# Kernel optimization log

Measured on AMD Instinct MI355X. Metric: run time of the kernel, lower is better.

The kernel has to match this reference:

```python
import jax, jax.numpy as jnp
import numpy as np

ALPHA = 0.2  # leakyrelu negative slope
NEG_INF = -1.0e12


def setup_inputs() -> dict:
    key = jax.random.key(0)
    k1, k2, k3, k4, k5 = jax.random.split(key, 5)
    B, N, C_in, C_out = 8, 2048, 256, 256
    inp = jax.random.normal(k1, (B, N, C_in), dtype=jnp.float32)
    adj = jax.random.randint(k2, (N, N), 0, 2, dtype=jnp.int32)
    # xavier_uniform with gain=1.414 for (C_in, C_out)
    limit = 1.414 * np.sqrt(6.0 / (C_in + C_out))
    W1 = jax.random.uniform(k3, (C_in, C_out), jnp.float32, -limit, limit)
    W2 = jax.random.uniform(k4, (C_in, C_out), jnp.float32, -limit, limit)
    W3 = jax.random.uniform(k5, (C_in, C_out), jnp.float32, -limit, limit)
    return {"inp": inp, "adj": adj, "W1": W1, "W2": W2, "W3": W3}


def reference(inp, adj, W1, W2, W3):
    # inp: [B,N,Cin], adj: [N,N], W*: [Cin,Cout]
    h1 = jnp.einsum('bnc,cd->bnd', inp, W1)  # [B,N,Cout] queries
    h2 = jnp.einsum('bnc,cd->bnd', inp, W2)  # [B,N,Cout] keys
    h3 = jnp.einsum('bnc,cd->bnd', inp, W3)  # [B,N,Cout] values
    e = jnp.einsum('bnd,bmd->bnm', h1, h2)   # [B,N,N] scores
    e = jax.nn.leaky_relu(e, ALPHA)
    e = jnp.where(adj[None, :, :] > 0, e, NEG_INF)
    attention = jax.nn.softmax(e, axis=-1)   # dropout p=0 / eval mode -> identity
    h_prime = jnp.einsum('bnm,bmd->bnd', attention, h3)
    return jax.nn.relu(h_prime)  # concat=True
```

## Files before the change

### kernel.cpp

```cpp
#include <hip/hip_runtime.h>

typedef __bf16 bf16_t;
typedef __bf16 bf16x4 __attribute__((ext_vector_type(4)));
typedef __bf16 bf16x8 __attribute__((ext_vector_type(8)));
typedef float floatx4 __attribute__((ext_vector_type(4)));
typedef signed char i8_t;
typedef int intx4 __attribute__((ext_vector_type(4)));

__device__ inline void split_hl(float v, bf16_t& hi, bf16_t& lo) {
    hi = (bf16_t)v;
    lo = (bf16_t)(v - (float)hi);
}

__global__ void wtrans_kernel(const float* __restrict__ W1,
                              const float* __restrict__ W2,
                              const float* __restrict__ W3,
                              bf16_t* __restrict__ Wthi, bf16_t* __restrict__ Wtlo) {
    __shared__ float T[64 * 68];
    const int zi = blockIdx.z;
    const float* W = (zi == 0) ? W1 : ((zi == 1) ? W2 : W3);
    bf16_t* ohi = Wthi + zi * 256 * 256;
    bf16_t* olo = Wtlo + zi * 256 * 256;
    const int c0 = blockIdx.x * 64, d0 = blockIdx.y * 64;
    const int tid = threadIdx.x;
#pragma unroll
    for (int i = 0; i < 4; i++) {
        int idx = i * 256 + tid;
        int r = idx >> 4, c4 = (idx & 15) * 4;
        floatx4 v = *(const floatx4*)(W + (c0 + r) * 256 + d0 + c4);
        *(floatx4*)(&T[r * 68 + c4]) = v;
    }
    __syncthreads();
#pragma unroll
    for (int i = 0; i < 4; i++) {
        int idx = i * 256 + tid;
        int rd = idx & 63, cc4 = (idx >> 6) * 4;
        bf16x4 vh, vl;
#pragma unroll
        for (int ii = 0; ii < 4; ii++) {
            float v = T[(cc4 + ii) * 68 + rd];
            bf16_t h, l; split_hl(v, h, l);
            vh[ii] = h; vl[ii] = l;
        }
        *(bf16x4*)(ohi + (d0 + rd) * 256 + c0 + cc4) = vh;
        *(bf16x4*)(olo + (d0 + rd) * 256 + c0 + cc4) = vl;
    }
}

__global__ __launch_bounds__(256) void projadj_kernel(
    const float* __restrict__ X,
    const bf16_t* __restrict__ Wthi, const bf16_t* __restrict__ Wtlo,
    i8_t* __restrict__ Q8h, i8_t* __restrict__ Q8l, float* __restrict__ sqv,
    i8_t* __restrict__ K8h, i8_t* __restrict__ K8l, float* __restrict__ skv,
    bf16_t* __restrict__ H3t,
    const int* __restrict__ adj, unsigned* __restrict__ bits) {
    __shared__ bf16_t Xh[64 * 40], Xl[64 * 40];
    __shared__ bf16_t Wh[256 * 40], Wl[256 * 40];
    __shared__ float amS[2][64];

    const int tid = threadIdx.x;
    const int blk = blockIdx.x;
    if (blk < 512) {
        int id = blk * 256 + tid;
        const int* p = adj + (size_t)id * 32;
        unsigned wbits = 0;
#pragma unroll
        for (int j = 0; j < 32; j += 4) {
            int4 v = *(const int4*)(p + j);
            wbits |= (v.x > 0 ? 1u : 0u) << j;
            wbits |= (v.y > 0 ? 1u : 0u) << (j + 1);
            wbits |= (v.z > 0 ? 1u : 0u) << (j + 2);
            wbits |= (v.w > 0 ? 1u : 0u) << (j + 3);
        }
        bits[id] = wbits;
        return;
    }

    const int pblk = blk - 512;
    const int z = pblk >> 8;
    const int row0 = (pblk & 255) * 64;
    const int w = tid >> 6, lane = tid & 63;
    const int m = lane & 15, q = lane >> 4;
    const int wr = w >> 1, wc = w & 1;
    const bf16_t* Wzh = Wthi + z * 256 * 256;
    const bf16_t* Wzl = Wtlo + z * 256 * 256;

    floatx4 acc[16];
#pragma unroll
    for (int i = 0; i < 16; i++) acc[i] = (floatx4){0.f, 0.f, 0.f, 0.f};

    for (int c0 = 0; c0 < 256; c0 += 32) {
#pragma unroll
        for (int i = 0; i < 2; i++) {
            int idx = i * 256 + tid;
            int r = idx >> 3, c4 = (idx & 7) * 4;
            floatx4 v = *(const floatx4*)(X + (size_t)(row0 + r) * 256 + c0 + c4);
            bf16x4 vh, vl;
#pragma unroll
            for (int ii = 0; ii < 4; ii++) {
                bf16_t h, l; split_hl(v[ii], h, l);
                vh[ii] = h; vl[ii] = l;
            }
            *(bf16x4*)(&Xh[r * 40 + c4]) = vh;
            *(bf16x4*)(&Xl[r * 40 + c4]) = vl;
        }
#pragma unroll
        for (int i = 0; i < 4; i++) {
            int idx = i * 256 + tid;
            int d = idx >> 2, c8 = (idx & 3) * 8;
            *(bf16x8*)(&Wh[d * 40 + c8]) = *(const bf16x8*)(Wzh + d * 256 + c0 + c8);
            *(bf16x8*)(&Wl[d * 40 + c8]) = *(const bf16x8*)(Wzl + d * 256 + c0 + c8);
        }
        __syncthreads();
        bf16x8 ah[2], al[2];
#pragma unroll
        for (int rt = 0; rt < 2; rt++) {
            ah[rt] = *(const bf16x8*)(&Xh[(wr * 32 + rt * 16 + m) * 40 + q * 8]);
            al[rt] = *(const bf16x8*)(&Xl[(wr * 32 + rt * 16 + m) * 40 + q * 8]);
        }
#pragma unroll
        for (int ct = 0; ct < 8; ct++) {
            bf16x8 bh = *(const bf16x8*)(&Wh[(wc * 128 + ct * 16 + m) * 40 + q * 8]);
            bf16x8 bl = *(const bf16x8*)(&Wl[(wc * 128 + ct * 16 + m) * 40 + q * 8]);
#pragma unroll
            for (int rt = 0; rt < 2; rt++) {
                acc[rt * 8 + ct] = __builtin_amdgcn_mfma_f32_16x16x32_bf16(ah[rt], bh, acc[rt * 8 + ct], 0, 0, 0);
                acc[rt * 8 + ct] = __builtin_amdgcn_mfma_f32_16x16x32_bf16(ah[rt], bl, acc[rt * 8 + ct], 0, 0, 0);
                acc[rt * 8 + ct] = __builtin_amdgcn_mfma_f32_16x16x32_bf16(al[rt], bh, acc[rt * 8 + ct], 0, 0, 0);
            }
        }
        __syncthreads();
    }

    if (z < 2) {
        i8_t* Dh = (z == 0) ? Q8h : K8h;
        i8_t* Dl = (z == 0) ? Q8l : K8l;
        float* sv = (z == 0) ? sqv : skv;
        float am[2][4];
#pragma unroll
        for (int rt = 0; rt < 2; rt++)
#pragma unroll
            for (int r = 0; r < 4; r++) am[rt][r] = 0.f;
#pragma unroll
        for (int ct = 0; ct < 8; ct++)
#pragma unroll
            for (int rt = 0; rt < 2; rt++)
#pragma unroll
                for (int r = 0; r < 4; r++)
                    am[rt][r] = fmaxf(am[rt][r], fabsf(acc[rt * 8 + ct][r]));
#pragma unroll
        for (int off = 1; off < 16; off <<= 1)
#pragma unroll
            for (int rt = 0; rt < 2; rt++)
#pragma unroll
                for (int r = 0; r < 4; r++)
                    am[rt][r] = fmaxf(am[rt][r], __shfl_xor(am[rt][r], off, 64));
        if (m == 0) {
#pragma unroll
            for (int rt = 0; rt < 2; rt++)
#pragma unroll
                for (int r = 0; r < 4; r++)
                    amS[wc][wr * 32 + rt * 16 + q * 4 + r] = am[rt][r];
        }
        __syncthreads();
        float sc[2][4], inv[2][4];
#pragma unroll
        for (int rt = 0; rt < 2; rt++)
#pragma unroll
            for (int r = 0; r < 4; r++) {
                int row = wr * 32 + rt * 16 + q * 4 + r;
                float a = fmaxf(amS[0][row], amS[1][row]);
                sc[rt][r]  = (a > 0.f) ? a * (1.f / 127.f) : 1.f;
                inv[rt][r] = (a > 0.f) ? 127.f / a : 0.f;
            }
#pragma unroll
        for (int ct = 0; ct < 8; ct++)
#pragma unroll
            for (int rt = 0; rt < 2; rt++)
#pragma unroll
                for (int r = 0; r < 4; r++) {
                    float vq = acc[rt * 8 + ct][r] * inv[rt][r];
                    float qh = rintf(vq);
                    float ql = fminf(fmaxf(rintf((vq - qh) * 256.f), -127.f), 127.f);
                    int offo = (row0 + wr * 32 + rt * 16 + q * 4 + r) * 256 +
                               wc * 128 + ct * 16 + m;
                    Dh[offo] = (i8_t)(int)qh;
                    Dl[offo] = (i8_t)(int)ql;
                }
        if (m == 0 && wc == 0) {
#pragma unroll
            for (int rt = 0; rt < 2; rt++)
#pragma unroll
                for (int r = 0; r < 4; r++)
                    sv[row0 + wr * 32 + rt * 16 + q * 4 + r] = sc[rt][r];
        }
    } else {
#pragma unroll
        for (int ct = 0; ct < 8; ct++)
#pragma unroll
            for (int rt = 0; rt < 2; rt++)
#pragma unroll
                for (int r = 0; r < 4; r++) {
                    int token = row0 + wr * 32 + rt * 16 + q * 4 + r;
                    int b = token >> 11, n = token & 2047;
                    H3t[(size_t)(b * 256 + wc * 128 + ct * 16 + m) * 2048 + n] =
                        (bf16_t)acc[rt * 8 + ct][r];
                }
    }
}

#define K8SW(row, off) ((off) ^ (((row) & 7) << 4))
#define VSW(row, off)  ((off) ^ ((((row) >> 1) & 3) << 4))
__global__ __launch_bounds__(256, 2) void attn_kernel(
    const i8_t* __restrict__ Q8h, const i8_t* __restrict__ Q8l,
    const float* __restrict__ sqv,
    const i8_t* __restrict__ K8h, const i8_t* __restrict__ K8l,
    const float* __restrict__ skv,
    const bf16_t* __restrict__ H3t, const unsigned* __restrict__ adjbits,
    bf16_t* __restrict__ Opart, float* __restrict__ mpart, float* __restrict__ lpart,
    int klen) {
    __shared__ i8_t K8[2][32 * 256];
    __shared__ bf16_t Vl[256 * 32];
    __shared__ bf16_t Pl[4][16 * 32];

    const int nwg = (int)(gridDim.x * gridDim.y * gridDim.z);
    const int wgid = (int)(blockIdx.x + (blockIdx.y << 5) + (blockIdx.z << 8));
    const int nid = (wgid & 7) * (nwg >> 3) + (wgid >> 3);
    const int qb = nid & 31;
    const int b  = (nid >> 5) & 7;
    const int kz = nid >> 8;

    const int q0 = qb * 64;
    const int tid = threadIdx.x;
    const int w = tid >> 6, lane = tid & 63;
    const int m = lane & 15, q = lane >> 4;

    char* K8B0 = (char*)&K8[0][0];
    char* K8B1 = (char*)&K8[1][0];
    char* VlB  = (char*)&Vl[0];
    char* PlB  = (char*)&Pl[w][0];

    const i8_t* qrh = Q8h + (size_t)(b * 2048 + q0 + w * 16 + m) * 256;
    const i8_t* qrl = Q8l + (size_t)(b * 2048 + q0 + w * 16 + m) * 256;
    intx4 qh8[4], ql8[4];
#pragma unroll
    for (int ck = 0; ck < 4; ck++) {
        qh8[ck] = *(const intx4*)(qrh + ck * 64 + q * 16);
        ql8[ck] = *(const intx4*)(qrl + ck * 64 + q * 16);
    }
    float sq4[4];
#pragma unroll
    for (int r = 0; r < 4; r++) sq4[r] = sqv[b * 2048 + q0 + w * 16 + q * 4 + r];

    bf16x8 vones;
#pragma unroll
    for (int i = 0; i < 8; i++) vones[i] = (bf16_t)1.0f;

    float m_run[4];
#pragma unroll
    for (int r = 0; r < 4; r++) m_run[r] = -3.0e38f;
    floatx4 l_acc = (floatx4){0.f, 0.f, 0.f, 0.f};
    floatx4 o[16];
#pragma unroll
    for (int i = 0; i < 16; i++) o[i] = (floatx4){0.f, 0.f, 0.f, 0.f};

    const unsigned* bitrow[4];
#pragma unroll
    for (int r = 0; r < 4; r++)
        bitrow[r] = adjbits + (size_t)(q0 + w * 16 + q * 4 + r) * 64;

    intx4 rkh[2], rkl[2];
    bf16x8 rvv[4];
    float skt[2], skn[2];
    const int kbeg = kz * klen, kend = kbeg + klen;

#pragma unroll
    for (int i = 0; i < 2; i++) {
        int ci = i * 256 + tid;
        int kr = ci >> 4, cb = (ci & 15) * 16;
        rkh[i] = *(const intx4*)(K8h + (size_t)(b * 2048 + kbeg + kr) * 256 + cb);
        rkl[i] = *(const intx4*)(K8l + (size_t)(b * 2048 + kbeg + kr) * 256 + cb);
    }
#pragma unroll
    for (int i = 0; i < 4; i++) {
        int ci = i * 256 + tid;
        int d = ci >> 2, k8 = (ci & 3) * 8;
        rvv[i] = *(const bf16x8*)(H3t + (size_t)(b * 256 + d) * 2048 + kbeg + k8);
    }
    skt[0] = skv[b * 2048 + kbeg + m];
    skt[1] = skv[b * 2048 + kbeg + 16 + m];

    for (int k0 = kbeg; k0 < kend; k0 += 32) {
        __syncthreads();
#pragma unroll
        for (int i = 0; i < 2; i++) {
            int ci = i * 256 + tid;
            int kr = ci >> 4, cb = (ci & 15) * 16;
            *(intx4*)(K8B0 + K8SW(kr, kr * 256 + cb)) = rkh[i];
            *(intx4*)(K8B1 + K8SW(kr, kr * 256 + cb)) = rkl[i];
        }
#pragma unroll
        for (int i = 0; i < 4; i++) {
            int ci = i * 256 + tid;
            int d = ci >> 2, kb = (ci & 3) * 16;
            *(bf16x8*)(VlB + VSW(d, d * 64 + kb)) = rvv[i];
        }
        __syncthreads();
        if (k0 + 32 < kend) {
            int kn = k0 + 32;
#pragma unroll
            for (int i = 0; i < 2; i++) {
                int ci = i * 256 + tid;
                int kr = ci >> 4, cb = (ci & 15) * 16;
                rkh[i] = *(const intx4*)(K8h + (size_t)(b * 2048 + kn + kr) * 256 + cb);
                rkl[i] = *(const intx4*)(K8l + (size_t)(b * 2048 + kn + kr) * 256 + cb);
            }
#pragma unroll
            for (int i = 0; i < 4; i++) {
                int ci = i * 256 + tid;
                int d = ci >> 2, k8 = (ci & 3) * 8;
                rvv[i] = *(const bf16x8*)(H3t + (size_t)(b * 256 + d) * 2048 + kn + k8);
            }
            skn[0] = skv[b * 2048 + kn + m];
            skn[1] = skv[b * 2048 + kn + 16 + m];
        }

        float s[2][4];
#pragma unroll
        for (int t = 0; t < 2; t++) {
            intx4 ch = {0, 0, 0, 0}, cm = {0, 0, 0, 0};
            const int row = t * 16 + m;
#pragma unroll
            for (int ck = 0; ck < 4; ck++) {
                const int cb2 = ck * 64 + q * 16;
                intx4 kh = *(const intx4*)(K8B0 + K8SW(row, row * 256 + cb2));
                intx4 kl = *(const intx4*)(K8B1 + K8SW(row, row * 256 + cb2));
                ch = __builtin_amdgcn_mfma_i32_16x16x64_i8(qh8[ck], kh, ch, 0, 0, 0);
                cm = __builtin_amdgcn_mfma_i32_16x16x64_i8(qh8[ck], kl, cm, 0, 0, 0);
                cm = __builtin_amdgcn_mfma_i32_16x16x64_i8(ql8[ck], kh, cm, 0, 0, 0);
            }
#pragma unroll
            for (int r = 0; r < 4; r++)
                s[t][r] = fmaf((float)cm[r], 0.00390625f, (float)ch[r]) * (sq4[r] * skt[t]);
        }

        unsigned aw[4];
#pragma unroll
        for (int r = 0; r < 4; r++) aw[r] = bitrow[r][k0 >> 5];
        float p[2][4], tmax[4];
#pragma unroll
        for (int r = 0; r < 4; r++) tmax[r] = -3.0e38f;
#pragma unroll
        for (int t = 0; t < 2; t++)
#pragma unroll
            for (int r = 0; r < 4; r++) {
                float v = s[t][r];
                v = (v > 0.f) ? v : 0.2f * v;
                v = ((aw[r] >> (t * 16 + m)) & 1u) ? v : -1.0e12f;
                p[t][r] = v;
                tmax[r] = fmaxf(tmax[r], v);
            }
#pragma unroll
        for (int off = 1; off < 16; off <<= 1)
#pragma unroll
            for (int r = 0; r < 4; r++)
                tmax[r] = fmaxf(tmax[r], __shfl_xor(tmax[r], off, 64));

        int rise = 0;
        float mnew[4];
#pragma unroll
        for (int r = 0; r < 4; r++) {
            mnew[r] = fmaxf(m_run[r], tmax[r]);
            rise |= (mnew[r] > m_run[r]);
        }
        if (__any(rise)) {
#pragma unroll
            for (int r = 0; r < 4; r++) {
                float alpha = __expf(m_run[r] - mnew[r]);
                m_run[r] = mnew[r];
                l_acc[r] *= alpha;
#pragma unroll
                for (int nt = 0; nt < 16; nt++) o[nt][r] *= alpha;
            }
        }
#pragma unroll
        for (int t = 0; t < 2; t++)
#pragma unroll
            for (int r = 0; r < 4; r++)
                p[t][r] = __expf(p[t][r] - m_run[r]);

#pragma unroll
        for (int t = 0; t < 2; t++)
#pragma unroll
            for (int r = 0; r < 4; r++) {
                int row = q * 4 + r;
                *(bf16_t*)(PlB + VSW(row, row * 64 + (t * 16 + m) * 2)) = (bf16_t)p[t][r];
            }
        bf16x8 pf = *(const bf16x8*)(PlB + VSW(m, m * 64 + q * 16));

        l_acc = __builtin_amdgcn_mfma_f32_16x16x32_bf16(pf, vones, l_acc, 0, 0, 0);

#pragma unroll
        for (int nt = 0; nt < 16; nt++) {
            const int vr = nt * 16 + m;
            bf16x8 vf = *(const bf16x8*)(VlB + VSW(vr, vr * 64 + q * 16));
            o[nt] = __builtin_amdgcn_mfma_f32_16x16x32_bf16(pf, vf, o[nt], 0, 0, 0);
        }
        skt[0] = skn[0];
        skt[1] = skn[1];
    }

    const int rowg = kz * 16384 + b * 2048 + q0 + w * 16 + q * 4;
#pragma unroll
    for (int nt = 0; nt < 16; nt++)
#pragma unroll
        for (int r = 0; r < 4; r++)
            Opart[(size_t)(rowg + r) * 256 + nt * 16 + m] = (bf16_t)o[nt][r];
    if (m == 0) {
#pragma unroll
        for (int r = 0; r < 4; r++) {
            mpart[rowg + r] = m_run[r];
            lpart[rowg + r] = l_acc[r];
        }
    }
}

__global__ __launch_bounds__(256) void merge_kernel(
    const bf16_t* __restrict__ Opart, const float* __restrict__ mpart,
    const float* __restrict__ lpart, float* __restrict__ out, int S) {
    int gid = blockIdx.x * 256 + threadIdx.x;
    int row = gid >> 6, c4 = (gid & 63) * 4;
    float M = -3.0e38f;
    for (int s = 0; s < S; s++) M = fmaxf(M, mpart[s * 16384 + row]);
    float denom = 0.f;
    float4 acc = make_float4(0.f, 0.f, 0.f, 0.f);
    for (int s = 0; s < S; s++) {
        float sc = __expf(mpart[s * 16384 + row] - M);
        denom += lpart[s * 16384 + row] * sc;
        bf16x4 v = *(const bf16x4*)(Opart + ((size_t)(s * 16384 + row)) * 256 + c4);
        acc.x += (float)v[0] * sc; acc.y += (float)v[1] * sc;
        acc.z += (float)v[2] * sc; acc.w += (float)v[3] * sc;
    }
    float inv = 1.f / denom;
    float4 r;
    r.x = fmaxf(acc.x * inv, 0.f);
    r.y = fmaxf(acc.y * inv, 0.f);
    r.z = fmaxf(acc.z * inv, 0.f);
    r.w = fmaxf(acc.w * inv, 0.f);
    *(float4*)(out + (size_t)row * 256 + c4) = r;
}

extern "C" void kernel_launch(void* const* d_in, const int* in_sizes, int n_in,
                              void* d_out, int out_size, void* d_ws, size_t ws_size,
                              hipStream_t stream) {
    const float* X   = (const float*)d_in[0];
    const int*   adj = (const int*)d_in[1];
    const float* W1  = (const float*)d_in[2];
    const float* W2  = (const float*)d_in[3];
    const float* W3  = (const float*)d_in[4];
    float* out = (float*)d_out;

    char* ws = (char*)d_ws;
    i8_t* Q8h = (i8_t*)(ws + ((size_t)0 << 20));
    i8_t* Q8l = (i8_t*)(ws + ((size_t)4 << 20));
    i8_t* K8h = (i8_t*)(ws + ((size_t)8 << 20));
    i8_t* K8l = (i8_t*)(ws + ((size_t)12 << 20));
    bf16_t* H3t = (bf16_t*)(ws + ((size_t)16 << 20));
    float* sqv = (float*)(ws + ((size_t)24 << 20));
    float* skv = (float*)(ws + ((size_t)24 << 20) + 65536);
    size_t wt0 = ((size_t)24 << 20) + 131072;
    bf16_t* Wthi = (bf16_t*)(ws + wt0);
    bf16_t* Wtlo = (bf16_t*)(ws + wt0 + 393216);
    float* mpart = (float*)(ws + wt0);
    float* lpart = (float*)(ws + wt0 + 131072);
    unsigned* adjb = (unsigned*)(ws + wt0 + 786432);
    size_t opart_off = wt0 + 786432 + 524288;
    const size_t need2 = opart_off + (size_t)2 * 16384 * 256 * 2;

    int S = (ws_size >= need2) ? 2 : 1;
    bf16_t* Opart = (bf16_t*)(ws + opart_off);

    wtrans_kernel<<<dim3(4, 4, 3), 256, 0, stream>>>(W1, W2, W3, Wthi, Wtlo);
    projadj_kernel<<<1280, 256, 0, stream>>>(X, Wthi, Wtlo,
                                             Q8h, Q8l, sqv, K8h, K8l, skv, H3t,
                                             adj, adjb);
    attn_kernel<<<dim3(32, 8, S), 256, 0, stream>>>(Q8h, Q8l, sqv, K8h, K8l, skv,
                                                    H3t, adjb, Opart, mpart, lpart,
                                                    2048 / S);
    merge_kernel<<<4096, 256, 0, stream>>>(Opart, mpart, lpart, out, S);
}
```

Measured before the change: 218.4 us.

## Stage V-transpose through LDS and add lazy softmax max rescaling

The H3 projection output is no longer scattered as single bf16 stores into the transposed layout. Each block now writes its tile into a padded shared-memory buffer that aliases the GEMM staging area, then emits coalesced 8-byte row stores. Separately, the online softmax now rescales the running max and accumulators only when the tile max exceeds the running max by more than 8, which cuts exp and multiply work. The lazy-rescale threshold lets exp values reach up to e^8, which risks precision loss in the bf16 P values and the accumulators.

```diff
diff --git a/kernel.cpp b/kernel.cpp
--- a/kernel.cpp
+++ b/kernel.cpp
@@ -54,9 +54,12 @@
     i8_t* __restrict__ K8h, i8_t* __restrict__ K8l, float* __restrict__ skv,
     bf16_t* __restrict__ H3t,
     const int* __restrict__ adj, unsigned* __restrict__ bits) {
-    __shared__ bf16_t Xh[64 * 40], Xl[64 * 40];
-    __shared__ bf16_t Wh[256 * 40], Wl[256 * 40];
-    __shared__ float amS[2][64];
+    __shared__ __align__(16) char SM[51712];
+    bf16_t* Xh = (bf16_t*)(SM);
+    bf16_t* Xl = (bf16_t*)(SM + 5120);
+    bf16_t* Wh = (bf16_t*)(SM + 10240);
+    bf16_t* Wl = (bf16_t*)(SM + 30720);
+    float* amS = (float*)(SM + 51200);
 
     const int tid = threadIdx.x;
     const int blk = blockIdx.x;
@@ -160,7 +163,7 @@
             for (int rt = 0; rt < 2; rt++)
 #pragma unroll
                 for (int r = 0; r < 4; r++)
-                    amS[wc][wr * 32 + rt * 16 + q * 4 + r] = am[rt][r];
+                    amS[wc * 64 + wr * 32 + rt * 16 + q * 4 + r] = am[rt][r];
         }
         __syncthreads();
         float sc[2][4], inv[2][4];
@@ -169,7 +172,7 @@
 #pragma unroll
             for (int r = 0; r < 4; r++) {
                 int row = wr * 32 + rt * 16 + q * 4 + r;
-                float a = fmaxf(amS[0][row], amS[1][row]);
+                float a = fmaxf(amS[row], amS[64 + row]);
                 sc[rt][r]  = (a > 0.f) ? a * (1.f / 127.f) : 1.f;
                 inv[rt][r] = (a > 0.f) ? 127.f / a : 0.f;
             }
@@ -195,17 +198,29 @@
                     sv[row0 + wr * 32 + rt * 16 + q * 4 + r] = sc[rt][r];
         }
     } else {
+        char* VtB = SM;
 #pragma unroll
         for (int ct = 0; ct < 8; ct++)
 #pragma unroll
-            for (int rt = 0; rt < 2; rt++)
-#pragma unroll
-                for (int r = 0; r < 4; r++) {
-                    int token = row0 + wr * 32 + rt * 16 + q * 4 + r;
-                    int b = token >> 11, n = token & 2047;
-                    H3t[(size_t)(b * 256 + wc * 128 + ct * 16 + m) * 2048 + n] =
-                        (bf16_t)acc[rt * 8 + ct][r];
-                }
+            for (int rt = 0; rt < 2; rt++) {
+                int d = wc * 128 + ct * 16 + m;
+                int n0 = wr * 32 + rt * 16 + q * 4;
+                bf16x4 v4;
+#pragma unroll
+                for (int r = 0; r < 4; r++) v4[r] = (bf16_t)acc[rt * 8 + ct][r];
+                *(bf16x4*)(VtB + d * 136 + n0 * 2) = v4;
+            }
+        __syncthreads();
+        const int bb = row0 >> 11;
+        const int nbase = row0 & 2047;
+        bf16_t* Hrow = H3t + (size_t)bb * 256 * 2048 + nbase;
+#pragma unroll
+        for (int it = 0; it < 16; it++) {
+            int d = it * 16 + (tid >> 4);
+            int c8 = tid & 15;
+            bf16x4 v = *(const bf16x4*)(VtB + d * 136 + c8 * 8);
+            *(bf16x4*)(Hrow + (size_t)d * 2048 + c8 * 4) = v;
+        }
     }
 }
 
@@ -367,17 +382,15 @@
                 tmax[r] = fmaxf(tmax[r], __shfl_xor(tmax[r], off, 64));
 
         int rise = 0;
-        float mnew[4];
-#pragma unroll
-        for (int r = 0; r < 4; r++) {
-            mnew[r] = fmaxf(m_run[r], tmax[r]);
-            rise |= (mnew[r] > m_run[r]);
-        }
+#pragma unroll
+        for (int r = 0; r < 4; r++)
+            rise |= (tmax[r] > m_run[r] + 8.f);
         if (__any(rise)) {
 #pragma unroll
             for (int r = 0; r < 4; r++) {
-                float alpha = __expf(m_run[r] - mnew[r]);
-                m_run[r] = mnew[r];
+                float mnew = fmaxf(m_run[r], tmax[r]);
+                float alpha = __expf(m_run[r] - mnew);
+                m_run[r] = mnew;
                 l_acc[r] *= alpha;
 #pragma unroll
                 for (int nt = 0; nt < 16; nt++) o[nt][r] *= alpha;
```

After: 218.9 us. No clear change (+0.2%).
